# Kernel optimization log

Measured on AMD Instinct MI355X. Metric: run time of the kernel, lower is better.

## Reference

```python
import jax, jax.numpy as jnp
import numpy as np

B, T, I, H, A = 256, 512, 256, 512, 18


def setup_inputs() -> dict:
    key = jax.random.key(0)
    ks = jax.random.split(key, 8)
    s_ih = 1.0 / np.sqrt(H)
    x = jax.random.normal(ks[0], (B, T, I), dtype=jnp.float32)
    h0 = jnp.zeros((1, B, H), dtype=jnp.float32)
    lengths = jax.random.randint(ks[1], (B,), 1, T + 1, dtype=jnp.int32)
    # nn.RNN parameters (uniform(-1/sqrt(H), 1/sqrt(H)) like torch default)
    W_ih = jax.random.uniform(ks[2], (H, I), minval=-s_ih, maxval=s_ih, dtype=jnp.float32)
    W_hh = jax.random.uniform(ks[3], (H, H), minval=-s_ih, maxval=s_ih, dtype=jnp.float32)
    b_ih = jax.random.uniform(ks[4], (H,), minval=-s_ih, maxval=s_ih, dtype=jnp.float32)
    b_hh = jax.random.uniform(ks[5], (H,), minval=-s_ih, maxval=s_ih, dtype=jnp.float32)
    W_fc = jax.random.uniform(ks[6], (A, H), minval=-s_ih, maxval=s_ih, dtype=jnp.float32)
    b_fc = jax.random.uniform(ks[7], (A,), minval=-s_ih, maxval=s_ih, dtype=jnp.float32)
    return {"x": x, "h0": h0, "lengths": lengths, "W_ih": W_ih, "W_hh": W_hh,
            "b_ih": b_ih, "b_hh": b_hh, "W_fc": W_fc, "b_fc": b_fc}


def _rnn_padded(x, h0, lengths, W_ih, W_hh, b_ih, b_hh):
    # Elman RNN (tanh), batch_first, with packed-sequence semantics:
    # hidden only updates while t < length; outputs past length are zero-padded.
    # Precompute input projection for all steps: [B, T, H]
    proj = jnp.einsum('bti,hi->bth', x, W_ih) + b_ih + b_hh
    proj_t = jnp.swapaxes(proj, 0, 1)  # [T, B, H]
    t_idx = jnp.arange(T, dtype=lengths.dtype)

    def step(h, inp):
        p, t = inp
        mask = (t < lengths)[:, None]  # [B, 1]
        h_new = jnp.tanh(p + h @ W_hh.T)
        h = jnp.where(mask, h_new, h)
        out = jnp.where(mask, h_new, 0.0)  # zero padding past length
        return h, out

    _, outs = jax.lax.scan(step, h0[0], (proj_t, t_idx))  # outs: [T, B, H]
    return jnp.swapaxes(outs, 0, 1)  # [B, T, H]


def reference(x, h0, lengths, W_ih, W_hh, b_ih, b_hh, W_fc, b_fc):
    out = _rnn_padded(x, h0, lengths, W_ih, W_hh, b_ih, b_hh)  # [B, T, H]
    action_values = jnp.einsum('bth,ah->bta', out, W_fc) + b_fc  # [B, T, A]
    return action_values, lengths
```

## Files before the change

kernel.cpp:

```cpp
#include <hip/hip_runtime.h>
#include <hip/hip_bf16.h>

#define Bb 256
#define Tt 512
#define Ii 256
#define Hh 512
#define Aa 18

typedef __bf16 bf16x8 __attribute__((ext_vector_type(8)));
typedef unsigned short u16x8 __attribute__((ext_vector_type(8)));
typedef unsigned short u16x4 __attribute__((ext_vector_type(4)));
typedef float f32x4 __attribute__((ext_vector_type(4)));
typedef int i32x4 __attribute__((ext_vector_type(4)));

__device__ __forceinline__ unsigned short f2bf(float x) {
    unsigned u = __builtin_bit_cast(unsigned, x);
    u += 0x7FFFu + ((u >> 16) & 1u);
    return (unsigned short)(u >> 16);
}
__device__ __forceinline__ float bf2f(unsigned short h) {
    unsigned u = ((unsigned)h) << 16;
    return __builtin_bit_cast(float, u);
}

__device__ __forceinline__ f32x4 mfma_bf16(u16x8 a, u16x8 b, f32x4 c) {
    return __builtin_amdgcn_mfma_f32_16x16x32_bf16(
        __builtin_bit_cast(bf16x8, a), __builtin_bit_cast(bf16x8, b), c, 0, 0, 0);
}

__device__ __forceinline__ float tanh_fast(float x) {
    float e = __expf(2.0f * x);
    return 1.0f - 2.0f * __builtin_amdgcn_rcpf(1.0f + e);
}

#define QW_SCALE 2873.6819587417f


__global__ void k_misc(const float* __restrict__ b_ih, const float* __restrict__ b_hh,
                       const float* __restrict__ w_fc, const int* __restrict__ lengths,
                       float* __restrict__ bias, int* __restrict__ wfcfrag,
                       float* __restrict__ out_tail) {
    int tid = threadIdx.x;
    for (int h = tid; h < Hh; h += 256) bias[h] = b_ih[h] + b_hh[h];
    for (int idx = tid; idx < 1024; idx += 256) {
        int nt = idx >> 9, k8 = (idx >> 6) & 7, lane = idx & 63;
        int a = nt * 16 + (lane & 15);
        int kb = k8 * 64 + (lane >> 4) * 16;
        int q[16];
#pragma unroll
        for (int i = 0; i < 16; ++i) {
            int qi = 0;
            if (a < Aa) {
                qi = (int)rintf(w_fc[a * Hh + kb + i] * QW_SCALE);
                qi = min(127, max(-127, qi));
            }
            q[i] = qi & 0xFF;
        }
        i32x4 pk;
#pragma unroll
        for (int d = 0; d < 4; ++d)
            pk[d] = q[d*4] | (q[d*4+1] << 8) | (q[d*4+2] << 16) | (q[d*4+3] << 24);
        *((i32x4*)wfcfrag + idx) = pk;
    }
    if (tid < Bb) out_tail[tid] = (float)lengths[tid];
}

__global__ void k_cast_wih(const float* __restrict__ wih, unsigned short* __restrict__ wih_bf) {
    int idx = (blockIdx.x * 256 + threadIdx.x) * 4;
    float4 f = *(const float4*)(wih + idx);
    u16x4 r = { f2bf(f.x), f2bf(f.y), f2bf(f.z), f2bf(f.w) };
    *(u16x4*)(wih_bf + idx) = r;
}

__global__ void k_prep_whh(const float* __restrict__ whh, int* __restrict__ w1frag) {
    int idx = blockIdx.x * 256 + threadIdx.x;
    int lane = idx & 63, k8 = (idx >> 6) & 7, nt = (idx >> 9) & 3, w = idx >> 11;
    int row = w * 64 + nt * 16 + (lane & 15);
    int kb = k8 * 64 + (lane >> 4) * 16;
    const float* src = whh + row * Hh + kb;
    int q[16];
#pragma unroll
    for (int i = 0; i < 16; ++i) {
        int qi = (int)rintf(src[i] * QW_SCALE);
        qi = min(127, max(-127, qi));
        q[i] = qi & 0xFF;
    }
    i32x4 pk;
#pragma unroll
    for (int d = 0; d < 4; ++d)
        pk[d] = q[d*4] | (q[d*4+1] << 8) | (q[d*4+2] << 16) | (q[d*4+3] << 24);
    *((i32x4*)w1frag + idx) = pk;
}

__global__ void k_prefill(const float* __restrict__ b_fc, float* __restrict__ out) {
    long long base = ((long long)blockIdx.x * 256 + threadIdx.x) * 4;
    int r = (int)(base % Aa);
    float4 v;
    v.x = b_fc[r]; r = (r == Aa - 1) ? 0 : r + 1;
    v.y = b_fc[r]; r = (r == Aa - 1) ? 0 : r + 1;
    v.z = b_fc[r]; r = (r == Aa - 1) ? 0 : r + 1;
    v.w = b_fc[r];
    *(float4*)(out + base) = v;
}


__global__ __launch_bounds__(512, 2) void k_gemm_proj(
        const float* __restrict__ x, const unsigned short* __restrict__ wih_bf,
        const float* __restrict__ bias, const int* __restrict__ lengths,
        unsigned short* __restrict__ projsw) {
    const int mbase = blockIdx.x * 128;
    const int b = mbase >> 9, t0 = mbase & 511;
    if (t0 >= lengths[b]) return;
    __shared__ __align__(16) unsigned short As[128 * 40];
    __shared__ __align__(16) unsigned short Bs[512 * 40];
    const int tid = threadIdx.x;
    const int wave = tid >> 6, lane = tid & 63;
    const int wm = wave & 1, wn = wave >> 1;
    const int quad = lane >> 4, l15 = lane & 15;

    f32x4 acc[4][8];
    const f32x4 zz = {0.f, 0.f, 0.f, 0.f};
#pragma unroll
    for (int i = 0; i < 4; i++)
#pragma unroll
        for (int j = 0; j < 8; j++) acc[i][j] = zz;

    const int arow = tid >> 2, aq = tid & 3;
    const float* aptr = x + (mbase + arow) * Ii + aq * 8;
    const unsigned short* bptr = wih_bf + tid * Ii;

    for (int kb = 0; kb < Ii / 32; ++kb) {
        float4 f0 = *(const float4*)(aptr + kb * 32);
        float4 f1 = *(const float4*)(aptr + kb * 32 + 4);
        u16x8 a8 = { f2bf(f0.x), f2bf(f0.y), f2bf(f0.z), f2bf(f0.w),
                     f2bf(f1.x), f2bf(f1.y), f2bf(f1.z), f2bf(f1.w) };
        *(u16x8*)&As[arow * 40 + aq * 8] = a8;
#pragma unroll
        for (int j = 0; j < 4; j++) {
            u16x8 b8 = *(const u16x8*)(bptr + kb * 32 + j * 8);
            *(u16x8*)&Bs[tid * 40 + j * 8] = b8;
        }
        __syncthreads();
        u16x8 af[4], bfr[8];
#pragma unroll
        for (int mt = 0; mt < 4; mt++)
            af[mt] = *(const u16x8*)&As[(wm * 64 + mt * 16 + l15) * 40 + quad * 8];
#pragma unroll
        for (int nt = 0; nt < 8; nt++)
            bfr[nt] = *(const u16x8*)&Bs[(wn * 128 + nt * 16 + l15) * 40 + quad * 8];
#pragma unroll
        for (int mt = 0; mt < 4; mt++)
#pragma unroll
            for (int nt = 0; nt < 8; nt++)
                acc[mt][nt] = mfma_bf16(af[mt], bfr[nt], acc[mt][nt]);
        __syncthreads();
    }
    float bv[8];
#pragma unroll
    for (int gnt = 0; gnt < 8; ++gnt) bv[gnt] = bias[wn * 128 + gnt * 16 + l15];
#pragma unroll
    for (int mt = 0; mt < 4; ++mt)
#pragma unroll
        for (int r2 = 0; r2 < 4; ++r2) {
            const int t = t0 + wm * 64 + mt * 16 + quad * 4 + r2;
            unsigned short* dst = projsw + ((size_t)(b * Tt + t)) * Hh + l15 * 4;
#pragma unroll
            for (int wv = 0; wv < 2; ++wv) {
                u16x4 v;
#pragma unroll
                for (int nt = 0; nt < 4; ++nt)
                    v[nt] = f2bf(acc[mt][wv * 4 + nt][r2] + bv[wv * 4 + nt]);
                *(u16x4*)(dst + (wn * 2 + wv) * 64) = v;
            }
        }
}


__global__ __launch_bounds__(512, 2) void k_rnn(
        const unsigned short* __restrict__ projsw, const int* __restrict__ w1frag,
        const int* __restrict__ wfcfrag, const float* __restrict__ b_fc,
        const int* __restrict__ lengths, float* __restrict__ out) {
    const int b = blockIdx.x;
    const int tid = threadIdx.x, w = tid >> 6, lane = tid & 63;
    const int quad = lane >> 4, l15 = lane & 15;
    __shared__ __align__(16) char hbuf[2][512];

    const int len = lengths[b];

    i32x4 wf[4][8];
    {
        const i32x4* wsrc = (const i32x4*)w1frag;
#pragma unroll
        for (int nt = 0; nt < 4; ++nt)
#pragma unroll
            for (int k8 = 0; k8 < 8; ++k8)
                wf[nt][k8] = wsrc[((w * 4 + nt) * 8 + k8) * 64 + lane];
    }
    const i32x4 zz = {0, 0, 0, 0};
    i32x4 wfc8[8];
#pragma unroll
    for (int k8 = 0; k8 < 8; ++k8) wfc8[k8] = zz;
    float bfc_r = 0.f;
    const int adim = w * 16 + l15;
    const bool a_ok = (w == 0) || (w == 1 && l15 < 2);
    if (w < 2) {
        const i32x4* fsrc = (const i32x4*)wfcfrag;
#pragma unroll
        for (int k8 = 0; k8 < 8; ++k8) wfc8[k8] = fsrc[(w * 8 + k8) * 64 + lane];
        if (a_ok) bfc_r = b_fc[adim];
    }

    const float C1 = 1.0f / (QW_SCALE * 127.0f);
    float* const obase = out + (size_t)b * Tt * Aa + adim;
    const unsigned short* pp = projsw + (size_t)b * Tt * Hh + (w * 64 + l15 * 4 + quad);

    auto step = [&](int t, unsigned short cv) {
        i32x4 a0 = zz, a1 = zz, a2 = zz, a3 = zz, aA = zz;
        if (t > 0) {
            const char* rb = hbuf[(t - 1) & 1];
#pragma unroll
            for (int k8 = 0; k8 < 8; ++k8) {
                i32x4 af = *(const i32x4*)(rb + k8 * 64 + quad * 16);
                a0 = __builtin_amdgcn_mfma_i32_16x16x64_i8(af, wf[0][k8], a0, 0, 0, 0);
                a1 = __builtin_amdgcn_mfma_i32_16x16x64_i8(af, wf[1][k8], a1, 0, 0, 0);
                a2 = __builtin_amdgcn_mfma_i32_16x16x64_i8(af, wf[2][k8], a2, 0, 0, 0);
                a3 = __builtin_amdgcn_mfma_i32_16x16x64_i8(af, wf[3][k8], a3, 0, 0, 0);
                if (w < 2)
                    aA = __builtin_amdgcn_mfma_i32_16x16x64_i8(af, wfc8[k8], aA, 0, 0, 0);
            }
        }
        int sel = a3[0];
        sel = (quad == 2) ? a2[0] : sel;
        sel = (quad == 1) ? a1[0] : sel;
        sel = (quad == 0) ? a0[0] : sel;
        const float hv = tanh_fast(bf2f(cv) + C1 * (float)sel);
        const int q = (int)rintf(hv * 127.0f);
        hbuf[t & 1][w * 64 + quad * 16 + l15] = (char)q;
        if (w < 2 && t > 0 && quad == 0 && a_ok)
            obase[(size_t)(t - 1) * Aa] = C1 * (float)aA[0] + bfc_r;
        asm volatile("s_waitcnt lgkmcnt(0)\n\ts_barrier" ::: "memory");
    };

    unsigned short c0 = pp[0];
    unsigned short c1 = pp[(size_t)((len > 1) ? 1 : 0) * Hh];
    int t = 0;
    for (; t + 1 < len; t += 2) {
        const int tp2 = (t + 2 < len) ? (t + 2) : (len - 1);
        const int tp3 = (t + 3 < len) ? (t + 3) : (len - 1);
        const unsigned short f0 = pp[(size_t)tp2 * Hh];
        const unsigned short f1 = pp[(size_t)tp3 * Hh];
        step(t, c0);
        step(t + 1, c1);
        c0 = f0; c1 = f1;
    }
    if (t < len) step(t, c0);

    if (w < 2) {
        const char* rb = hbuf[(len - 1) & 1];
        i32x4 aA = zz;
#pragma unroll
        for (int k8 = 0; k8 < 8; ++k8) {
            i32x4 af = *(const i32x4*)(rb + k8 * 64 + quad * 16);
            aA = __builtin_amdgcn_mfma_i32_16x16x64_i8(af, wfc8[k8], aA, 0, 0, 0);
        }
        if (quad == 0 && a_ok)
            obase[(size_t)(len - 1) * Aa] = C1 * (float)aA[0] + bfc_r;
    }
}


extern "C" void kernel_launch(void* const* d_in, const int* in_sizes, int n_in,
                              void* d_out, int out_size, void* d_ws, size_t ws_size,
                              hipStream_t stream) {
    const float* x       = (const float*)d_in[0];
    const int*   lengths = (const int*)d_in[2];
    const float* wih     = (const float*)d_in[3];
    const float* whh     = (const float*)d_in[4];
    const float* bih     = (const float*)d_in[5];
    const float* bhh     = (const float*)d_in[6];
    const float* wfc     = (const float*)d_in[7];
    const float* bfc     = (const float*)d_in[8];
    float* out = (float*)d_out;
    char* ws = (char*)d_ws;

    const size_t OFF_PROJ  = 0;
    const size_t OFF_WIH   = OFF_PROJ + 134217728ull;
    const size_t OFF_W1    = OFF_WIH + 262144;
    const size_t OFF_WFCF  = OFF_W1 + 262144;
    const size_t OFF_BIAS  = OFF_WFCF + 16384;

    unsigned short* projsw  = (unsigned short*)(ws + OFF_PROJ);
    unsigned short* wih_bf  = (unsigned short*)(ws + OFF_WIH);
    int*            w1frag  = (int*)(ws + OFF_W1);
    int*            wfcfrag = (int*)(ws + OFF_WFCF);
    float* bias             = (float*)(ws + OFF_BIAS);

    k_misc<<<1, 256, 0, stream>>>(bih, bhh, wfc, lengths, bias, wfcfrag,
                                  out + (size_t)Bb * Tt * Aa);
    k_cast_wih<<<128, 256, 0, stream>>>(wih, wih_bf);
    k_prep_whh<<<64, 256, 0, stream>>>(whh, w1frag);
    k_prefill<<<2304, 256, 0, stream>>>(bfc, out);
    k_gemm_proj<<<1024, 512, 0, stream>>>(x, wih_bf, bias, lengths, projsw);
    k_rnn<<<Bb, 512, 0, stream>>>(projsw, w1frag, wfcfrag, bfc, lengths, out);
}
```

Before: 695.0 us.

## Split recurrent matvec across MFMA and sdot4, distribute FC head over waves

In the RNN kernel, the fourth recurrent MFMA tile per wave is replaced by per-lane sdot4 dot products reduced with cross-lane shuffles. The output FC projection is now split across all eight waves with shared-memory partial sums, reduced one step later by a single wave, so waves 0-1 no longer carry the extra MFMA chain. This is meant to shorten the serial per-timestep critical path. It also adds a register-prefetch of the next K-slice in the projection GEMM, at the cost of more shared memory, a new weight layout, and extra shuffle/reduction work.

```diff
diff --git a/kernel.cpp b/kernel.cpp
--- a/kernel.cpp
+++ b/kernel.cpp
@@ -7,6 +7,12 @@
 #define Hh 512
 #define Aa 18
 
+#if __has_builtin(__builtin_amdgcn_sdot4)
+#define HAS_SDOT4 1
+#else
+#define HAS_SDOT4 0
+#endif
+
 typedef __bf16 bf16x8 __attribute__((ext_vector_type(8)));
 typedef unsigned short u16x8 __attribute__((ext_vector_type(8)));
 typedef unsigned short u16x4 __attribute__((ext_vector_type(4)));
@@ -27,6 +33,7 @@
     return __builtin_amdgcn_mfma_f32_16x16x32_bf16(
         __builtin_bit_cast(bf16x8, a), __builtin_bit_cast(bf16x8, b), c, 0, 0, 0);
 }
+#define MFMA8(a, b, c) __builtin_amdgcn_mfma_i32_16x16x64_i8((a), (b), (c), 0, 0, 0)
 
 __device__ __forceinline__ float tanh_fast(float x) {
     float e = __expf(2.0f * x);
@@ -72,12 +79,25 @@
     *(u16x4*)(wih_bf + idx) = r;
 }
 
-__global__ void k_prep_whh(const float* __restrict__ whh, int* __restrict__ w1frag) {
+__global__ void k_prep_whh(const float* __restrict__ whh, int* __restrict__ w1frag,
+                           int* __restrict__ wdotfrag) {
     int idx = blockIdx.x * 256 + threadIdx.x;
-    int lane = idx & 63, k8 = (idx >> 6) & 7, nt = (idx >> 9) & 3, w = idx >> 11;
-    int row = w * 64 + nt * 16 + (lane & 15);
-    int kb = k8 * 64 + (lane >> 4) * 16;
-    const float* src = whh + row * Hh + kb;
+    const float* src;
+    int* dst;
+    if (idx < 16384) {
+        int lane = idx & 63, k8 = (idx >> 6) & 7, nt = (idx >> 9) & 3, w = idx >> 11;
+        int row = w * 64 + nt * 16 + (lane & 15);
+        int kb = k8 * 64 + (lane >> 4) * 16;
+        src = whh + row * Hh + kb;
+        dst = (int*)((i32x4*)w1frag + idx);
+    } else {
+        int i2 = idx - 16384;
+        int lane = i2 & 63, k8 = (i2 >> 6) & 7, g = i2 >> 9;
+        int col = g * 64 + 48 + (lane & 15);
+        int kb = k8 * 64 + (lane >> 4) * 16;
+        src = whh + col * Hh + kb;
+        dst = (int*)((i32x4*)wdotfrag + i2);
+    }
     int q[16];
 #pragma unroll
     for (int i = 0; i < 16; ++i) {
@@ -89,7 +109,7 @@
 #pragma unroll
     for (int d = 0; d < 4; ++d)
         pk[d] = q[d*4] | (q[d*4+1] << 8) | (q[d*4+2] << 16) | (q[d*4+3] << 24);
-    *((i32x4*)w1frag + idx) = pk;
+    *(i32x4*)dst = pk;
 }
 
 __global__ void k_prefill(const float* __restrict__ b_fc, float* __restrict__ out) {
@@ -129,18 +149,30 @@
     const float* aptr = x + (mbase + arow) * Ii + aq * 8;
     const unsigned short* bptr = wih_bf + tid * Ii;
 
+    float4 f0 = *(const float4*)(aptr);
+    float4 f1 = *(const float4*)(aptr + 4);
+    u16x8 bs0 = *(const u16x8*)(bptr);
+    u16x8 bs1 = *(const u16x8*)(bptr + 8);
+    u16x8 bs2 = *(const u16x8*)(bptr + 16);
+    u16x8 bs3 = *(const u16x8*)(bptr + 24);
+
     for (int kb = 0; kb < Ii / 32; ++kb) {
-        float4 f0 = *(const float4*)(aptr + kb * 32);
-        float4 f1 = *(const float4*)(aptr + kb * 32 + 4);
         u16x8 a8 = { f2bf(f0.x), f2bf(f0.y), f2bf(f0.z), f2bf(f0.w),
                      f2bf(f1.x), f2bf(f1.y), f2bf(f1.z), f2bf(f1.w) };
         *(u16x8*)&As[arow * 40 + aq * 8] = a8;
-#pragma unroll
-        for (int j = 0; j < 4; j++) {
-            u16x8 b8 = *(const u16x8*)(bptr + kb * 32 + j * 8);
-            *(u16x8*)&Bs[tid * 40 + j * 8] = b8;
-        }
+        *(u16x8*)&Bs[tid * 40]      = bs0;
+        *(u16x8*)&Bs[tid * 40 + 8]  = bs1;
+        *(u16x8*)&Bs[tid * 40 + 16] = bs2;
+        *(u16x8*)&Bs[tid * 40 + 24] = bs3;
         __syncthreads();
+        if (kb < Ii / 32 - 1) {
+            f0 = *(const float4*)(aptr + (kb + 1) * 32);
+            f1 = *(const float4*)(aptr + (kb + 1) * 32 + 4);
+            bs0 = *(const u16x8*)(bptr + (kb + 1) * 32);
+            bs1 = *(const u16x8*)(bptr + (kb + 1) * 32 + 8);
+            bs2 = *(const u16x8*)(bptr + (kb + 1) * 32 + 16);
+            bs3 = *(const u16x8*)(bptr + (kb + 1) * 32 + 24);
+        }
         u16x8 af[4], bfr[8];
 #pragma unroll
         for (int mt = 0; mt < 4; mt++)
@@ -178,66 +210,112 @@
 
 __global__ __launch_bounds__(512, 2) void k_rnn(
         const unsigned short* __restrict__ projsw, const int* __restrict__ w1frag,
-        const int* __restrict__ wfcfrag, const float* __restrict__ b_fc,
-        const int* __restrict__ lengths, float* __restrict__ out) {
+        const int* __restrict__ wfcfrag, const int* __restrict__ wdotfrag,
+        const float* __restrict__ b_fc, const int* __restrict__ lengths,
+        float* __restrict__ out) {
     const int b = blockIdx.x;
     const int tid = threadIdx.x, w = tid >> 6, lane = tid & 63;
     const int quad = lane >> 4, l15 = lane & 15;
     __shared__ __align__(16) char hbuf[2][512];
+    __shared__ int fcpart[2][8][32];
 
     const int len = lengths[b];
-
-    i32x4 wf[4][8];
+    const i32x4 zz = {0, 0, 0, 0};
+
+#if HAS_SDOT4
+#define NT_MFMA 3
+#else
+#define NT_MFMA 4
+#endif
+    i32x4 wf[NT_MFMA][8];
     {
         const i32x4* wsrc = (const i32x4*)w1frag;
 #pragma unroll
-        for (int nt = 0; nt < 4; ++nt)
+        for (int nt = 0; nt < NT_MFMA; ++nt)
 #pragma unroll
             for (int k8 = 0; k8 < 8; ++k8)
                 wf[nt][k8] = wsrc[((w * 4 + nt) * 8 + k8) * 64 + lane];
     }
-    const i32x4 zz = {0, 0, 0, 0};
-    i32x4 wfc8[8];
-#pragma unroll
-    for (int k8 = 0; k8 < 8; ++k8) wfc8[k8] = zz;
-    float bfc_r = 0.f;
-    const int adim = w * 16 + l15;
-    const bool a_ok = (w == 0) || (w == 1 && l15 < 2);
-    if (w < 2) {
+#if HAS_SDOT4
+    i32x4 wd[8];
+    {
+        const i32x4* dsrc = (const i32x4*)wdotfrag;
+#pragma unroll
+        for (int k8 = 0; k8 < 8; ++k8)
+            wd[k8] = dsrc[(w * 8 + k8) * 64 + lane];
+    }
+#endif
+    i32x4 wfcs[2];
+    {
         const i32x4* fsrc = (const i32x4*)wfcfrag;
-#pragma unroll
-        for (int k8 = 0; k8 < 8; ++k8) wfc8[k8] = fsrc[(w * 8 + k8) * 64 + lane];
-        if (a_ok) bfc_r = b_fc[adim];
-    }
+        wfcs[0] = fsrc[(0 * 8 + w) * 64 + lane];
+        wfcs[1] = fsrc[(1 * 8 + w) * 64 + lane];
+    }
+    const bool red = (w == 7) && (lane < 32);
+    const int adim = ((lane >> 4) & 1) * 16 + l15;
+    const bool a_ok = red && (adim < Aa);
+    const float bfc_r = a_ok ? b_fc[adim] : 0.f;
+    float* const obase = out + (size_t)b * Tt * Aa + adim;
 
     const float C1 = 1.0f / (QW_SCALE * 127.0f);
-    float* const obase = out + (size_t)b * Tt * Aa + adim;
     const unsigned short* pp = projsw + (size_t)b * Tt * Hh + (w * 64 + l15 * 4 + quad);
 
     auto step = [&](int t, unsigned short cv) {
-        i32x4 a0 = zz, a1 = zz, a2 = zz, a3 = zz, aA = zz;
+        i32x4 a0 = zz, a1 = zz, a2 = zz;
+#if HAS_SDOT4
+        int ad = 0;
+#else
+        i32x4 a3 = zz;
+#endif
         if (t > 0) {
             const char* rb = hbuf[(t - 1) & 1];
+            i32x4 af[8];
+#pragma unroll
+            for (int k8 = 0; k8 < 8; ++k8)
+                af[k8] = *(const i32x4*)(rb + k8 * 64 + quad * 16);
 #pragma unroll
             for (int k8 = 0; k8 < 8; ++k8) {
-                i32x4 af = *(const i32x4*)(rb + k8 * 64 + quad * 16);
-                a0 = __builtin_amdgcn_mfma_i32_16x16x64_i8(af, wf[0][k8], a0, 0, 0, 0);
-                a1 = __builtin_amdgcn_mfma_i32_16x16x64_i8(af, wf[1][k8], a1, 0, 0, 0);
-                a2 = __builtin_amdgcn_mfma_i32_16x16x64_i8(af, wf[2][k8], a2, 0, 0, 0);
-                a3 = __builtin_amdgcn_mfma_i32_16x16x64_i8(af, wf[3][k8], a3, 0, 0, 0);
-                if (w < 2)
-                    aA = __builtin_amdgcn_mfma_i32_16x16x64_i8(af, wfc8[k8], aA, 0, 0, 0);
+                a0 = MFMA8(af[k8], wf[0][k8], a0);
+                a1 = MFMA8(af[k8], wf[1][k8], a1);
+                a2 = MFMA8(af[k8], wf[2][k8], a2);
+#if HAS_SDOT4
+#pragma unroll
+                for (int e = 0; e < 4; ++e)
+                    ad = __builtin_amdgcn_sdot4(af[k8][e], wd[k8][e], ad, false);
+#else
+                a3 = MFMA8(af[k8], wf[3][k8], a3);
+#endif
             }
-        }
+            i32x4 afw = *(const i32x4*)(rb + w * 64 + quad * 16);
+            i32x4 aF0 = MFMA8(afw, wfcs[0], zz);
+            i32x4 aF1 = MFMA8(afw, wfcs[1], zz);
+#if HAS_SDOT4
+            ad += __shfl_xor(ad, 16);
+            ad += __shfl_xor(ad, 32);
+#endif
+            if (quad == 0) {
+                fcpart[t & 1][w][l15]      = aF0[0];
+                fcpart[t & 1][w][16 + l15] = aF1[0];
+            }
+            if (red && t >= 2) {
+                const int* fp = &fcpart[(t - 1) & 1][0][0];
+                int s = 0;
+#pragma unroll
+                for (int kw = 0; kw < 8; ++kw) s += fp[kw * 32 + lane];
+                if (a_ok) obase[(size_t)(t - 2) * Aa] = C1 * (float)s + bfc_r;
+            }
+        }
+#if HAS_SDOT4
+        int sel = ad;
+#else
         int sel = a3[0];
+#endif
         sel = (quad == 2) ? a2[0] : sel;
         sel = (quad == 1) ? a1[0] : sel;
         sel = (quad == 0) ? a0[0] : sel;
         const float hv = tanh_fast(bf2f(cv) + C1 * (float)sel);
         const int q = (int)rintf(hv * 127.0f);
         hbuf[t & 1][w * 64 + quad * 16 + l15] = (char)q;
-        if (w < 2 && t > 0 && quad == 0 && a_ok)
-            obase[(size_t)(t - 1) * Aa] = C1 * (float)aA[0] + bfc_r;
         asm volatile("s_waitcnt lgkmcnt(0)\n\ts_barrier" ::: "memory");
     };
 
@@ -255,16 +333,30 @@
     }
     if (t < len) step(t, c0);
 
-    if (w < 2) {
-        const char* rb = hbuf[(len - 1) & 1];
-        i32x4 aA = zz;
-#pragma unroll
-        for (int k8 = 0; k8 < 8; ++k8) {
-            i32x4 af = *(const i32x4*)(rb + k8 * 64 + quad * 16);
-            aA = __builtin_amdgcn_mfma_i32_16x16x64_i8(af, wfc8[k8], aA, 0, 0, 0);
-        }
-        if (quad == 0 && a_ok)
-            obase[(size_t)(len - 1) * Aa] = C1 * (float)aA[0] + bfc_r;
+    {
+        const char* rbT = hbuf[(len - 1) & 1];
+        i32x4 afw = *(const i32x4*)(rbT + w * 64 + quad * 16);
+        i32x4 aF0 = MFMA8(afw, wfcs[0], zz);
+        i32x4 aF1 = MFMA8(afw, wfcs[1], zz);
+        if (quad == 0) {
+            fcpart[len & 1][w][l15]      = aF0[0];
+            fcpart[len & 1][w][16 + l15] = aF1[0];
+        }
+    }
+    asm volatile("s_waitcnt lgkmcnt(0)\n\ts_barrier" ::: "memory");
+    if (red) {
+        if (len >= 2) {
+            const int* fp = &fcpart[(len - 1) & 1][0][0];
+            int s = 0;
+#pragma unroll
+            for (int kw = 0; kw < 8; ++kw) s += fp[kw * 32 + lane];
+            if (a_ok) obase[(size_t)(len - 2) * Aa] = C1 * (float)s + bfc_r;
+        }
+        const int* fp2 = &fcpart[len & 1][0][0];
+        int s2 = 0;
+#pragma unroll
+        for (int kw = 0; kw < 8; ++kw) s2 += fp2[kw * 32 + lane];
+        if (a_ok) obase[(size_t)(len - 1) * Aa] = C1 * (float)s2 + bfc_r;
     }
 }
 
@@ -287,19 +379,22 @@
     const size_t OFF_WIH   = OFF_PROJ + 134217728ull;
     const size_t OFF_W1    = OFF_WIH + 262144;
     const size_t OFF_WFCF  = OFF_W1 + 262144;
-    const size_t OFF_BIAS  = OFF_WFCF + 16384;
+    const size_t OFF_WDOT  = OFF_WFCF + 16384;
+    const size_t OFF_BIAS  = OFF_WDOT + 65536;
 
     unsigned short* projsw  = (unsigned short*)(ws + OFF_PROJ);
     unsigned short* wih_bf  = (unsigned short*)(ws + OFF_WIH);
     int*            w1frag  = (int*)(ws + OFF_W1);
     int*            wfcfrag = (int*)(ws + OFF_WFCF);
+    int*            wdotfrag= (int*)(ws + OFF_WDOT);
     float* bias             = (float*)(ws + OFF_BIAS);
 
     k_misc<<<1, 256, 0, stream>>>(bih, bhh, wfc, lengths, bias, wfcfrag,
                                   out + (size_t)Bb * Tt * Aa);
     k_cast_wih<<<128, 256, 0, stream>>>(wih, wih_bf);
-    k_prep_whh<<<64, 256, 0, stream>>>(whh, w1frag);
+    k_prep_whh<<<80, 256, 0, stream>>>(whh, w1frag, wdotfrag);
     k_prefill<<<2304, 256, 0, stream>>>(bfc, out);
     k_gemm_proj<<<1024, 512, 0, stream>>>(x, wih_bf, bias, lengths, projsw);
-    k_rnn<<<Bb, 512, 0, stream>>>(projsw, w1frag, wfcfrag, bfc, lengths, out);
-}
+    k_rnn<<<Bb, 512, 0, stream>>>(projsw, w1frag, wfcfrag, wdotfrag, bfc,
+                                  lengths, out);
+}
```

Result: slower. 730.3 us (+5.1%).

## Split FC projection across waves and start recurrence MFMAs from own h slice

Applied to the files above, without the earlier changes.

In the RNN kernel, the output FC projection no longer runs only on waves 0-1. Each wave now computes a partial FC product over its own k-slice of h. Those partial sums go to shared memory and wave 7 reduces them one step later. Each wave also keeps its own freshly written h fragment in registers and rotates its k-order so the first MFMA needs no LDS read. This shortens the per-step critical path and balances load across waves, at the cost of extra LDS traffic, a delayed reduction and more complex tail handling. The projection GEMM also gets register prefetch of the next K tile's global loads, to overlap load latency with MFMA work.

```diff
diff --git a/kernel.cpp b/kernel.cpp
--- a/kernel.cpp
+++ b/kernel.cpp
@@ -27,6 +27,7 @@
     return __builtin_amdgcn_mfma_f32_16x16x32_bf16(
         __builtin_bit_cast(bf16x8, a), __builtin_bit_cast(bf16x8, b), c, 0, 0, 0);
 }
+#define MFMA8(a, b, c) __builtin_amdgcn_mfma_i32_16x16x64_i8((a), (b), (c), 0, 0, 0)
 
 __device__ __forceinline__ float tanh_fast(float x) {
     float e = __expf(2.0f * x);
@@ -129,18 +130,30 @@
     const float* aptr = x + (mbase + arow) * Ii + aq * 8;
     const unsigned short* bptr = wih_bf + tid * Ii;
 
+    float4 f0 = *(const float4*)(aptr);
+    float4 f1 = *(const float4*)(aptr + 4);
+    u16x8 bs0 = *(const u16x8*)(bptr);
+    u16x8 bs1 = *(const u16x8*)(bptr + 8);
+    u16x8 bs2 = *(const u16x8*)(bptr + 16);
+    u16x8 bs3 = *(const u16x8*)(bptr + 24);
+
     for (int kb = 0; kb < Ii / 32; ++kb) {
-        float4 f0 = *(const float4*)(aptr + kb * 32);
-        float4 f1 = *(const float4*)(aptr + kb * 32 + 4);
         u16x8 a8 = { f2bf(f0.x), f2bf(f0.y), f2bf(f0.z), f2bf(f0.w),
                      f2bf(f1.x), f2bf(f1.y), f2bf(f1.z), f2bf(f1.w) };
         *(u16x8*)&As[arow * 40 + aq * 8] = a8;
-#pragma unroll
-        for (int j = 0; j < 4; j++) {
-            u16x8 b8 = *(const u16x8*)(bptr + kb * 32 + j * 8);
-            *(u16x8*)&Bs[tid * 40 + j * 8] = b8;
-        }
+        *(u16x8*)&Bs[tid * 40]      = bs0;
+        *(u16x8*)&Bs[tid * 40 + 8]  = bs1;
+        *(u16x8*)&Bs[tid * 40 + 16] = bs2;
+        *(u16x8*)&Bs[tid * 40 + 24] = bs3;
         __syncthreads();
+        if (kb < Ii / 32 - 1) {
+            f0 = *(const float4*)(aptr + (kb + 1) * 32);
+            f1 = *(const float4*)(aptr + (kb + 1) * 32 + 4);
+            bs0 = *(const u16x8*)(bptr + (kb + 1) * 32);
+            bs1 = *(const u16x8*)(bptr + (kb + 1) * 32 + 8);
+            bs2 = *(const u16x8*)(bptr + (kb + 1) * 32 + 16);
+            bs3 = *(const u16x8*)(bptr + (kb + 1) * 32 + 24);
+        }
         u16x8 af[4], bfr[8];
 #pragma unroll
         for (int mt = 0; mt < 4; mt++)
@@ -184,87 +197,120 @@
     const int tid = threadIdx.x, w = tid >> 6, lane = tid & 63;
     const int quad = lane >> 4, l15 = lane & 15;
     __shared__ __align__(16) char hbuf[2][512];
+    __shared__ int fcpart[2][8][32];
 
     const int len = lengths[b];
+    const i32x4 zz = {0, 0, 0, 0};
 
     i32x4 wf[4][8];
+    int koff[8];
     {
         const i32x4* wsrc = (const i32x4*)w1frag;
 #pragma unroll
-        for (int nt = 0; nt < 4; ++nt)
-#pragma unroll
-            for (int k8 = 0; k8 < 8; ++k8)
-                wf[nt][k8] = wsrc[((w * 4 + nt) * 8 + k8) * 64 + lane];
-    }
-    const i32x4 zz = {0, 0, 0, 0};
-    i32x4 wfc8[8];
-#pragma unroll
-    for (int k8 = 0; k8 < 8; ++k8) wfc8[k8] = zz;
-    float bfc_r = 0.f;
-    const int adim = w * 16 + l15;
-    const bool a_ok = (w == 0) || (w == 1 && l15 < 2);
-    if (w < 2) {
+        for (int j = 0; j < 8; ++j) {
+            const int k8p = (w + j) & 7;
+            koff[j] = k8p * 64 + quad * 16;
+#pragma unroll
+            for (int nt = 0; nt < 4; ++nt)
+                wf[nt][j] = wsrc[((w * 4 + nt) * 8 + k8p) * 64 + lane];
+        }
+    }
+    i32x4 wfcs[2];
+    {
         const i32x4* fsrc = (const i32x4*)wfcfrag;
-#pragma unroll
-        for (int k8 = 0; k8 < 8; ++k8) wfc8[k8] = fsrc[(w * 8 + k8) * 64 + lane];
-        if (a_ok) bfc_r = b_fc[adim];
-    }
+        wfcs[0] = fsrc[(0 * 8 + w) * 64 + lane];
+        wfcs[1] = fsrc[(1 * 8 + w) * 64 + lane];
+    }
+    const bool red = (w == 7) && (lane < 32);
+    const bool a_ok = red && (lane < Aa);
+    const float bfc_r = a_ok ? b_fc[lane] : 0.f;
+    float* const obase = out + (size_t)b * Tt * Aa + lane;
 
     const float C1 = 1.0f / (QW_SCALE * 127.0f);
-    float* const obase = out + (size_t)b * Tt * Aa + adim;
+    const int hoff = w * 64 + quad * 16 + l15;
+    const int ownoff = w * 64 + quad * 16;
     const unsigned short* pp = projsw + (size_t)b * Tt * Hh + (w * 64 + l15 * 4 + quad);
 
-    auto step = [&](int t, unsigned short cv) {
-        i32x4 a0 = zz, a1 = zz, a2 = zz, a3 = zz, aA = zz;
-        if (t > 0) {
-            const char* rb = hbuf[(t - 1) & 1];
-#pragma unroll
-            for (int k8 = 0; k8 < 8; ++k8) {
-                i32x4 af = *(const i32x4*)(rb + k8 * 64 + quad * 16);
-                a0 = __builtin_amdgcn_mfma_i32_16x16x64_i8(af, wf[0][k8], a0, 0, 0, 0);
-                a1 = __builtin_amdgcn_mfma_i32_16x16x64_i8(af, wf[1][k8], a1, 0, 0, 0);
-                a2 = __builtin_amdgcn_mfma_i32_16x16x64_i8(af, wf[2][k8], a2, 0, 0, 0);
-                a3 = __builtin_amdgcn_mfma_i32_16x16x64_i8(af, wf[3][k8], a3, 0, 0, 0);
-                if (w < 2)
-                    aA = __builtin_amdgcn_mfma_i32_16x16x64_i8(af, wfc8[k8], aA, 0, 0, 0);
-            }
-        }
+    i32x4 af_own;
+    {
+        const float hv = tanh_fast(bf2f(pp[0]));
+        const int q = (int)rintf(hv * 127.0f);
+        hbuf[0][hoff] = (char)q;
+        asm volatile("s_waitcnt lgkmcnt(0)" ::: "memory");
+        af_own = *(const i32x4*)(&hbuf[0][0] + ownoff);
+        asm volatile("s_barrier" ::: "memory");
+    }
+
+    unsigned short cv = (len > 1) ? pp[Hh] : (unsigned short)0;
+    for (int t = 1; t < len; ++t) {
+        const unsigned short nv = pp[(size_t)((t + 1 < len) ? t + 1 : len - 1) * Hh];
+        const char* rb = &hbuf[(t - 1) & 1][0];
+        char* wb = &hbuf[t & 1][0];
+
+        int rsum = 0;
+        const bool do_red = red && (t >= 2);
+        if (do_red) {
+            const int* fp = &fcpart[t & 1][0][0];
+#pragma unroll
+            for (int kw = 0; kw < 8; ++kw) rsum += fp[kw * 32 + lane];
+        }
+
+        i32x4 a0 = MFMA8(af_own, wf[0][0], zz);
+        i32x4 a1 = MFMA8(af_own, wf[1][0], zz);
+        i32x4 a2 = MFMA8(af_own, wf[2][0], zz);
+        i32x4 a3 = MFMA8(af_own, wf[3][0], zz);
+        i32x4 aF0 = MFMA8(af_own, wfcs[0], zz);
+        i32x4 aF1 = MFMA8(af_own, wfcs[1], zz);
+#pragma unroll
+        for (int j = 1; j < 8; ++j) {
+            const i32x4 af = *(const i32x4*)(rb + koff[j]);
+            a0 = MFMA8(af, wf[0][j], a0);
+            a1 = MFMA8(af, wf[1][j], a1);
+            a2 = MFMA8(af, wf[2][j], a2);
+            a3 = MFMA8(af, wf[3][j], a3);
+        }
+        if (quad == 0) {
+            fcpart[(t - 1) & 1][w][l15]      = aF0[0];
+            fcpart[(t - 1) & 1][w][16 + l15] = aF1[0];
+        }
+        if (do_red && a_ok)
+            obase[(size_t)(t - 2) * Aa] = C1 * (float)rsum + bfc_r;
+
         int sel = a3[0];
         sel = (quad == 2) ? a2[0] : sel;
         sel = (quad == 1) ? a1[0] : sel;
         sel = (quad == 0) ? a0[0] : sel;
         const float hv = tanh_fast(bf2f(cv) + C1 * (float)sel);
         const int q = (int)rintf(hv * 127.0f);
-        hbuf[t & 1][w * 64 + quad * 16 + l15] = (char)q;
-        if (w < 2 && t > 0 && quad == 0 && a_ok)
-            obase[(size_t)(t - 1) * Aa] = C1 * (float)aA[0] + bfc_r;
-        asm volatile("s_waitcnt lgkmcnt(0)\n\ts_barrier" ::: "memory");
-    };
-
-    unsigned short c0 = pp[0];
-    unsigned short c1 = pp[(size_t)((len > 1) ? 1 : 0) * Hh];
-    int t = 0;
-    for (; t + 1 < len; t += 2) {
-        const int tp2 = (t + 2 < len) ? (t + 2) : (len - 1);
-        const int tp3 = (t + 3 < len) ? (t + 3) : (len - 1);
-        const unsigned short f0 = pp[(size_t)tp2 * Hh];
-        const unsigned short f1 = pp[(size_t)tp3 * Hh];
-        step(t, c0);
-        step(t + 1, c1);
-        c0 = f0; c1 = f1;
-    }
-    if (t < len) step(t, c0);
-
-    if (w < 2) {
-        const char* rb = hbuf[(len - 1) & 1];
-        i32x4 aA = zz;
-#pragma unroll
-        for (int k8 = 0; k8 < 8; ++k8) {
-            i32x4 af = *(const i32x4*)(rb + k8 * 64 + quad * 16);
-            aA = __builtin_amdgcn_mfma_i32_16x16x64_i8(af, wfc8[k8], aA, 0, 0, 0);
-        }
-        if (quad == 0 && a_ok)
-            obase[(size_t)(len - 1) * Aa] = C1 * (float)aA[0] + bfc_r;
+        wb[hoff] = (char)q;
+        asm volatile("s_waitcnt lgkmcnt(0)" ::: "memory");
+        af_own = *(const i32x4*)(wb + ownoff);
+        asm volatile("s_barrier" ::: "memory");
+        cv = nv;
+    }
+
+    {
+        i32x4 aF0 = MFMA8(af_own, wfcs[0], zz);
+        i32x4 aF1 = MFMA8(af_own, wfcs[1], zz);
+        if (quad == 0) {
+            fcpart[(len - 1) & 1][w][l15]      = aF0[0];
+            fcpart[(len - 1) & 1][w][16 + l15] = aF1[0];
+        }
+    }
+    asm volatile("s_waitcnt lgkmcnt(0)\n\ts_barrier" ::: "memory");
+    if (red) {
+        if (len >= 2) {
+            const int* fp = &fcpart[(len - 2) & 1][0][0];
+            int s = 0;
+#pragma unroll
+            for (int kw = 0; kw < 8; ++kw) s += fp[kw * 32 + lane];
+            if (a_ok) obase[(size_t)(len - 2) * Aa] = C1 * (float)s + bfc_r;
+        }
+        const int* fp2 = &fcpart[(len - 1) & 1][0][0];
+        int s2 = 0;
+#pragma unroll
+        for (int kw = 0; kw < 8; ++kw) s2 += fp2[kw * 32 + lane];
+        if (a_ok) obase[(size_t)(len - 1) * Aa] = C1 * (float)s2 + bfc_r;
     }
 }
 
```

New measurement: 684.3 us. No clear change (-1.5%).
